# Optimization experiments

Hardware: AMD Instinct MI355X
Metric: run time of the kernel (lower is better)

## Reference

```python
import jax, jax.numpy as jnp
import numpy as np

NUM_HEADS = 16


def _rope(x, c, s):
    # x: [T, H, D]; c, s: [T, D/2] -> rotate-half RoPE over full head_dim
    d2 = c.shape[-1]
    x1, x2 = x[..., :d2], x[..., d2:]
    c = c[:, None, :]
    s = s[:, None, :]
    return jnp.concatenate([x1 * c - x2 * s, x2 * c + x1 * s], axis=-1)


def setup_inputs() -> dict:
    key = jax.random.key(0)
    ks = jax.random.split(key, 4)
    B, L, dim = 8, 1024, 1024
    T = B * L
    D = dim // NUM_HEADS
    hidden_states = jax.random.normal(ks[0], (T, dim), dtype=jnp.float32)
    w_qkv = jax.random.normal(ks[1], (dim, 3 * dim), dtype=jnp.float32) * (dim ** -0.5)
    b_qkv = jnp.zeros((3 * dim,), dtype=jnp.float32)
    w_proj = jax.random.normal(ks[2], (dim, dim), dtype=jnp.float32) * (dim ** -0.5)
    b_proj = jnp.zeros((dim,), dtype=jnp.float32)
    # RoPE tables: positions restart at 0 for each packed sequence
    pos = jnp.tile(jnp.arange(L, dtype=jnp.float32), B)  # [T]
    inv_freq = 1.0 / (10000.0 ** (jnp.arange(0, D, 2, dtype=jnp.float32) / D))  # [D/2]
    freqs = pos[:, None] * inv_freq[None, :]  # [T, D/2]
    emb = jnp.concatenate([freqs, freqs], axis=-1)  # [T, D]
    cos = jnp.cos(emb)
    sin = jnp.sin(emb)
    cu_seqlens = (jnp.arange(B + 1, dtype=jnp.int32) * L)
    return {"hidden_states": hidden_states, "cos": cos, "sin": sin,
            "w_qkv": w_qkv, "b_qkv": b_qkv, "w_proj": w_proj, "b_proj": b_proj,
            "cu_seqlens": cu_seqlens}


def reference(hidden_states, cos, sin, w_qkv, b_qkv, w_proj, b_proj, cu_seqlens):
    T, dim = hidden_states.shape
    H = NUM_HEADS
    D = dim // H
    B = cu_seqlens.shape[0] - 1  # equal-length packed sequences
    L = T // B

    qkv = hidden_states @ w_qkv + b_qkv            # [T, 3*dim]
    qkv = qkv.reshape(T, 3, H, D)
    q, k, v = qkv[:, 0], qkv[:, 1], qkv[:, 2]       # [T, H, D]

    # module chunks cos/sin in half along last dim before apply_rotary_emb
    c = cos[..., : D // 2].astype(jnp.float32)
    s = sin[..., : D // 2].astype(jnp.float32)
    q = _rope(q.astype(jnp.float32), c, s).astype(hidden_states.dtype)
    k = _rope(k.astype(jnp.float32), c, s).astype(hidden_states.dtype)

    # varlen flash attention == block-diagonal attention; equal lengths -> reshape
    qb = q.reshape(B, L, H, D)
    kb = k.reshape(B, L, H, D)
    vb = v.reshape(B, L, H, D)
    scale = D ** -0.5
    scores = jnp.einsum("bqhd,bkhd->bhqk", qb, kb) * scale  # [B, H, L, L]
    probs = jax.nn.softmax(scores, axis=-1)
    out = jnp.einsum("bhqk,bkhd->bqhd", probs, vb)           # [B, L, H, D]
    out = out.reshape(T, dim)
    return out @ w_proj + b_proj
```

## Files before the change

### kernel.cpp

```cpp
#include <hip/hip_runtime.h>

typedef unsigned short ushort_t;
typedef __attribute__((ext_vector_type(8))) short short8;
typedef __attribute__((ext_vector_type(4))) float f32x4;

#define AS1 __attribute__((address_space(1)))
#define AS3 __attribute__((address_space(3)))

__device__ __forceinline__ ushort_t f2bf(float f) {
  unsigned int u = __builtin_bit_cast(unsigned int, f);
  u += 0x7fffu + ((u >> 16) & 1u);
  return (ushort_t)(u >> 16);
}

__device__ __forceinline__ unsigned int pack_bf2(float a, float b) {
  unsigned int ua = __builtin_bit_cast(unsigned int, a) + 0x8000u;
  unsigned int ub = __builtin_bit_cast(unsigned int, b) + 0x8000u;
  return (ua >> 16) | (ub & 0xffff0000u);
}

#if defined(__has_builtin)
#if __has_builtin(__builtin_amdgcn_cvt_pk_bf16_f32)
#define HAVE_CVT_PK_BF16 1
#endif
#if __has_builtin(__builtin_amdgcn_exp2f)
#define HAVE_EXP2 1
#endif
#endif

__device__ __forceinline__ unsigned int pack2(float a, float b) {
#ifdef HAVE_CVT_PK_BF16
  typedef __attribute__((ext_vector_type(2))) __bf16 bf2_t;
  bf2_t r = __builtin_amdgcn_cvt_pk_bf16_f32(a, b);
  return __builtin_bit_cast(unsigned int, r);
#else
  return pack_bf2(a, b);
#endif
}

__device__ __forceinline__ float fast_exp2(float x) {
#ifdef HAVE_EXP2
  return __builtin_amdgcn_exp2f(x);
#else
  return exp2f(x);
#endif
}

__device__ __forceinline__ void load_lds16(const ushort_t* g, ushort_t* l) {
  __builtin_amdgcn_global_load_lds((AS1 void*)g, (AS3 void*)l, 16, 0, 0);
}

#define MFMA16(a, b, c) __builtin_amdgcn_mfma_f32_16x16x32_bf16((a), (b), (c), 0, 0, 0)

__global__ __launch_bounds__(256) void k_prep(const float* __restrict__ hs,
                                              ushort_t* __restrict__ hsb,
                                              const float* __restrict__ wqkv,
                                              ushort_t* __restrict__ wqkvT,
                                              const float* __restrict__ wproj,
                                              ushort_t* __restrict__ wprojT) {
  __shared__ __align__(16) ushort_t t[64 * 66];
  const int bid = blockIdx.x;
  if (bid < 4096) {
    int i = bid * 256 + threadIdx.x;
    const float4* s4 = (const float4*)hs;
    float4 a = s4[(size_t)i * 2], b = s4[(size_t)i * 2 + 1];
    short8 o;
    o[0] = (short)f2bf(a.x); o[1] = (short)f2bf(a.y);
    o[2] = (short)f2bf(a.z); o[3] = (short)f2bf(a.w);
    o[4] = (short)f2bf(b.x); o[5] = (short)f2bf(b.y);
    o[6] = (short)f2bf(b.z); o[7] = (short)f2bf(b.w);
    *(short8*)(hsb + (size_t)i * 8) = o;
    return;
  }
  const float* src;
  ushort_t* dst;
  int C, bx, by;
  if (bid < 4864) { int idx = bid - 4096; src = wqkv; dst = wqkvT; C = 3072;
                    bx = idx % 48; by = idx / 48; }
  else            { int idx = bid - 4864; src = wproj; dst = wprojT; C = 1024;
                    bx = idx & 15; by = idx >> 4; }
  const int R = 1024;
  const int x0 = bx * 64, y0 = by * 64;
  const int a2 = threadIdx.x & 31;
  const int r0 = threadIdx.x >> 5;
#pragma unroll
  for (int i = 0; i < 8; ++i) {
    int r = r0 + i * 8;
    float2 v = *(const float2*)&src[(size_t)(y0 + r) * C + x0 + 2 * a2];
    t[(2 * a2) * 66 + r]     = f2bf(v.x);
    t[(2 * a2 + 1) * 66 + r] = f2bf(v.y);
  }
  __syncthreads();
#pragma unroll
  for (int i = 0; i < 8; ++i) {
    int rr = r0 + i * 8;
    unsigned int w = *(const unsigned int*)&t[rr * 66 + 2 * a2];
    *(unsigned int*)&dst[(size_t)(x0 + rr) * R + y0 + 2 * a2] = w;
  }
}

__global__ __launch_bounds__(512) void k_qkv_gemm_rope(
    const ushort_t* __restrict__ A, const ushort_t* __restrict__ Bt,
    const float* __restrict__ bias, const float* __restrict__ cosb,
    const float* __restrict__ sinb, ushort_t* __restrict__ Qb,
    ushort_t* __restrict__ Kb, ushort_t* __restrict__ Vp) {
  constexpr int K = 1024;
  __shared__ __align__(16) ushort_t As[256 * 64];
  __shared__ __align__(16) ushort_t Bs[128 * 64];
  const int tid = threadIdx.x, lane = tid & 63, wave = tid >> 6;
  const int quad = lane >> 4, ml = lane & 15;
  const int wm = wave & 3, wn = wave >> 2;
  const int L = blockIdx.x, xcd = L & 7, j = L >> 3;
  const int by = xcd * 4 + j / 24, bx = j % 24;
  const int m0 = by * 256, n0 = bx * 128;
  f32x4 acc[4][4] = {};

  for (int kt = 0; kt < K / 64; ++kt) {
    __syncthreads();
    {
      const int kk0 = kt * 64;
#pragma unroll
      for (int i = 0; i < 4; ++i) {
        int cch = i * 512 + tid;
        int r = cch >> 3, s = cch & 7, gs = s ^ (r & 7);
        load_lds16(A + (size_t)(m0 + r) * K + kk0 + gs * 8, As + cch * 8);
      }
#pragma unroll
      for (int i = 0; i < 2; ++i) {
        int cch = i * 512 + tid;
        int r = cch >> 3, s = cch & 7, gs = s ^ (r & 7);
        load_lds16(Bt + (size_t)(n0 + r) * K + kk0 + gs * 8, Bs + cch * 8);
      }
    }
    __syncthreads();
#pragma unroll
    for (int ks = 0; ks < 2; ++ks) {
      short8 af[4], bfr[4];
#pragma unroll
      for (int mb = 0; mb < 4; ++mb) {
        int row = wm * 64 + mb * 16 + ml;
        int gs = (ks * 4 + quad) ^ (row & 7);
        af[mb] = *(const short8*)(As + row * 64 + gs * 8);
      }
#pragma unroll
      for (int nb = 0; nb < 4; ++nb) {
        int row = wn * 64 + nb * 16 + ml;
        int gs = (ks * 4 + quad) ^ (row & 7);
        bfr[nb] = *(const short8*)(Bs + row * 64 + gs * 8);
      }
#pragma unroll
      for (int mb = 0; mb < 4; ++mb)
#pragma unroll
        for (int nb = 0; nb < 4; ++nb)
          acc[mb][nb] = MFMA16(af[mb], bfr[nb], acc[mb][nb]);
    }
  }

  const int ncol0 = n0 + wn * 64;
  const int sec = ncol0 >> 10;
  const int h = (ncol0 & 1023) >> 6;
  if (sec < 2) {
    ushort_t* dst = (sec == 0) ? Qb : Kb;
    const float qs = (sec == 0) ? 0.18033688011112042f : 1.0f;
#pragma unroll
    for (int mb = 0; mb < 4; ++mb) {
#pragma unroll
      for (int rg = 0; rg < 4; ++rg) {
        const int m = m0 + wm * 64 + mb * 16 + quad * 4 + rg;
        const int b = m >> 10, l = m & 1023;
        const size_t ob = ((size_t)(b * 16 + h) * 1024 + l) * 64;
#pragma unroll
        for (int nb = 0; nb < 2; ++nb) {
          const int d = nb * 16 + ml;
          float x1 = acc[mb][nb][rg] + bias[ncol0 + d];
          float x2 = acc[mb][nb + 2][rg] + bias[ncol0 + d + 32];
          float cv = cosb[(size_t)m * 64 + d] * qs;
          float sv = sinb[(size_t)m * 64 + d] * qs;
          dst[ob + d] = f2bf(x1 * cv - x2 * sv);
          dst[ob + d + 32] = f2bf(x2 * cv + x1 * sv);
        }
      }
    }
  } else {
    const int mrow = m0 + wm * 64;
    const int b = mrow >> 10, lB = mrow & 1023;
    ushort_t* vb = Vp + ((size_t)(b * 16 + h)) * 65536 + lB;
#pragma unroll
    for (int rg = 0; rg < 4; ++rg) {
#pragma unroll
      for (int nb = 0; nb < 4; ++nb) {
        const int d = nb * 16 + ml;
        const float bs = bias[ncol0 + d];
        uint2 w;
        w.x = pack_bf2(acc[0][nb][rg] + bs, acc[1][nb][rg] + bs);
        w.y = pack_bf2(acc[2][nb][rg] + bs, acc[3][nb][rg] + bs);
        *(uint2*)(vb + (size_t)d * 1024 + 16 * quad + 4 * rg) = w;
      }
    }
  }
}

__global__ __launch_bounds__(512, 4) void k_attn(const ushort_t* __restrict__ Qb,
                                                 const ushort_t* __restrict__ Kb,
                                                 const ushort_t* __restrict__ Vp,
                                                 ushort_t* __restrict__ Ob) {
  __shared__ __align__(16) ushort_t S[32768];
  const int tid = threadIdx.x, lane = tid & 63, wave = tid >> 6;
  const int quad = lane >> 4, ml = lane & 15;
  const int bh = blockIdx.x & 127, qt = blockIdx.x >> 7;
  const int q0 = qt * 256;
  const size_t base = (size_t)bh * 65536;

#pragma unroll
  for (int i = 0; i < 4; ++i) {
    int cch = i * 512 + tid;
    int r = cch >> 3, s = cch & 7, gs = s ^ (r & 7);
    load_lds16(Qb + base + (size_t)(q0 + r) * 64 + gs * 8, S + cch * 8);
  }

  const ushort_t* kg;
  const ushort_t* vg;
  ushort_t *kl, *vl;
  {
    int r = tid >> 3, gs = (tid & 7) ^ (r & 7);
    kg = Kb + base + (size_t)r * 64 + gs * 8;
    kl = S + 16384 + tid * 8;
    vg = Vp + base + (size_t)r * 1024 + gs * 8;
    vl = S + 24576 + tid * 8;
  }
  load_lds16(kg, kl); kg += 4096;
  load_lds16(vg, vl); vg += 64;
  __syncthreads();

  const int gsA = quad ^ (ml & 7);
  const int gsB = (4 + quad) ^ (ml & 7);
  const int h0 = (ml >> 1) ^ (quad * 4);

  short8 qf[2][2];
#pragma unroll
  for (int mb = 0; mb < 2; ++mb) {
    int rowoff = wave * 2048 + mb * 1024 + ml * 64;
    qf[mb][0] = *(const short8*)(S + rowoff + gsA * 8);
    qf[mb][1] = *(const short8*)(S + rowoff + gsB * 8);
  }
  __syncthreads();

  const ushort_t* kA = S + 16384 + ml * 64 + gsA * 8;
  const ushort_t* kB = S + 16384 + ml * 64 + gsB * 8;
  const ushort_t* pA = S + wave * 2048 + ml * 64 + gsA * 8;
  const ushort_t* pB = S + wave * 2048 + ml * 64 + gsB * 8;
  ushort_t* pwl = S + wave * 2048 + quad * 256 + (ml & 1) * 4;

  f32x4 Oacc[2][4] = {};
  float lsum[2][4] = {};

#define ATTN_STEP(CUR, LAST)                                                  \
  {                                                                           \
    if (!(LAST)) {                                                            \
      load_lds16(kg, kl + ((CUR) ^ 1) * 4096); kg += 4096;                    \
      load_lds16(vg, vl + ((CUR) ^ 1) * 4096); vg += 64;                      \
    }                                                                         \
    f32x4 Sacc[2][4] = {};                                                    \
    __builtin_amdgcn_s_setprio(1);                                            \
    _Pragma("unroll") for (int nb = 0; nb < 4; ++nb) {                        \
      short8 kfa = *(const short8*)(kA + (CUR) * 4096 + nb * 1024);           \
      short8 kfb = *(const short8*)(kB + (CUR) * 4096 + nb * 1024);           \
      Sacc[0][nb] = MFMA16(qf[0][0], kfa, Sacc[0][nb]);                       \
      Sacc[1][nb] = MFMA16(qf[1][0], kfa, Sacc[1][nb]);                       \
      Sacc[0][nb] = MFMA16(qf[0][1], kfb, Sacc[0][nb]);                       \
      Sacc[1][nb] = MFMA16(qf[1][1], kfb, Sacc[1][nb]);                       \
    }                                                                         \
    __builtin_amdgcn_s_setprio(0);                                            \
    _Pragma("unroll") for (int mb = 0; mb < 2; ++mb) {                        \
      _Pragma("unroll") for (int rg = 0; rg < 4; ++rg) {                      \
        float p0 = fast_exp2(Sacc[mb][0][rg]);                                \
        float p1 = fast_exp2(Sacc[mb][1][rg]);                                \
        float p2 = fast_exp2(Sacc[mb][2][rg]);                                \
        float p3 = fast_exp2(Sacc[mb][3][rg]);                                \
        lsum[mb][rg] += (p0 + p1) + (p2 + p3);                                \
        uint2 w;                                                              \
        w.x = pack2(p0, p1);                                                  \
        w.y = pack2(p2, p3);                                                  \
        int g8 = ((h0 ^ rg) & 7) * 8;                                         \
        *(uint2*)(pwl + mb * 1024 + rg * 64 + g8) = w;                        \
      }                                                                       \
    }                                                                         \
    __builtin_amdgcn_s_setprio(1);                                            \
    _Pragma("unroll") for (int ks = 0; ks < 2; ++ks) {                        \
      const ushort_t* pk = ks ? pB : pA;                                      \
      const ushort_t* vk = (ks ? kB : kA) + 8192 + (CUR) * 4096;              \
      short8 pf0 = *(const short8*)(pk);                                      \
      short8 pf1 = *(const short8*)(pk + 1024);                               \
      _Pragma("unroll") for (int nb = 0; nb < 4; ++nb) {                      \
        short8 vf = *(const short8*)(vk + nb * 1024);                         \
        Oacc[0][nb] = MFMA16(pf0, vf, Oacc[0][nb]);                           \
        Oacc[1][nb] = MFMA16(pf1, vf, Oacc[1][nb]);                           \
      }                                                                       \
    }                                                                         \
    __builtin_amdgcn_s_setprio(0);                                            \
    __syncthreads();                                                          \
  }

#pragma unroll 1
  for (int kt2 = 0; kt2 < 8; ++kt2) {
    ATTN_STEP(0, false)
    ATTN_STEP(1, kt2 == 7)
  }
#undef ATTN_STEP

  const int b = bh >> 4, h = bh & 15;
#pragma unroll
  for (int mb = 0; mb < 2; ++mb) {
#pragma unroll
    for (int rg = 0; rg < 4; ++rg) {
      float l = lsum[mb][rg];
      l += __shfl_xor(l, 1);
      l += __shfl_xor(l, 2);
      l += __shfl_xor(l, 4);
      l += __shfl_xor(l, 8);
      float inv = 1.f / l;
      int q = q0 + wave * 32 + mb * 16 + quad * 4 + rg;
      size_t ob = ((size_t)(b * 1024 + q)) * 1024 + h * 64;
#pragma unroll
      for (int nb = 0; nb < 4; ++nb)
        Ob[ob + nb * 16 + ml] = f2bf(Oacc[mb][nb][rg] * inv);
    }
  }
}

__global__ __launch_bounds__(256) void k_proj_gemm(const ushort_t* __restrict__ A,
                                                   const ushort_t* __restrict__ Bt,
                                                   const float* __restrict__ bias,
                                                   float* __restrict__ out) {
  constexpr int K = 1024;
  __shared__ __align__(16) ushort_t As[128 * 128];
  __shared__ __align__(16) ushort_t Bs[128 * 128];
  const int tid = threadIdx.x, lane = tid & 63, wave = tid >> 6;
  const int quad = lane >> 4, ml = lane & 15;
  const int wm = wave & 1, wn = wave >> 1;
  const int L = blockIdx.x, xcd = L & 7, j = L >> 3;
  const int by = xcd * 8 + (j >> 3), bx = j & 7;
  const int m0 = by * 128, n0 = bx * 128;
  f32x4 acc[4][4] = {};

  for (int kt = 0; kt < K / 128; ++kt) {
    __syncthreads();
    {
      const int kk0 = kt * 128;
#pragma unroll
      for (int i = 0; i < 8; ++i) {
        int cch = i * 256 + tid;
        int r = cch >> 4, s = cch & 15, gs = s ^ (r & 15);
        load_lds16(A + (size_t)(m0 + r) * K + kk0 + gs * 8, As + cch * 8);
        load_lds16(Bt + (size_t)(n0 + r) * K + kk0 + gs * 8, Bs + cch * 8);
      }
    }
    __syncthreads();
#pragma unroll
    for (int ks = 0; ks < 4; ++ks) {
      short8 af[4], bfr[4];
#pragma unroll
      for (int mb = 0; mb < 4; ++mb) {
        int row = wm * 64 + mb * 16 + ml;
        int gs = (ks * 4 + quad) ^ (row & 15);
        af[mb] = *(const short8*)(As + row * 128 + gs * 8);
      }
#pragma unroll
      for (int nb = 0; nb < 4; ++nb) {
        int row = wn * 64 + nb * 16 + ml;
        int gs = (ks * 4 + quad) ^ (row & 15);
        bfr[nb] = *(const short8*)(Bs + row * 128 + gs * 8);
      }
#pragma unroll
      for (int mb = 0; mb < 4; ++mb)
#pragma unroll
        for (int nb = 0; nb < 4; ++nb)
          acc[mb][nb] = MFMA16(af[mb], bfr[nb], acc[mb][nb]);
    }
  }
#pragma unroll
  for (int mb = 0; mb < 4; ++mb) {
#pragma unroll
    for (int rg = 0; rg < 4; ++rg) {
      const int m = m0 + wm * 64 + mb * 16 + quad * 4 + rg;
#pragma unroll
      for (int nb = 0; nb < 4; ++nb) {
        const int n = n0 + wn * 64 + nb * 16 + ml;
        out[(size_t)m * 1024 + n] = acc[mb][nb][rg] + bias[n];
      }
    }
  }
}

extern "C" void kernel_launch(void* const* d_in, const int* in_sizes, int n_in,
                              void* d_out, int out_size, void* d_ws, size_t ws_size,
                              hipStream_t stream) {
  const float* hs = (const float*)d_in[0];
  const float* cosb = (const float*)d_in[1];
  const float* sinb = (const float*)d_in[2];
  const float* wqkv = (const float*)d_in[3];
  const float* bqkv = (const float*)d_in[4];
  const float* wproj = (const float*)d_in[5];
  const float* bproj = (const float*)d_in[6];
  float* out = (float*)d_out;

  char* ws = (char*)d_ws;
  ushort_t* hsb = (ushort_t*)(ws);
  ushort_t* wqkvT = (ushort_t*)(ws + (16u << 20));
  ushort_t* wprojT = (ushort_t*)(ws + (22u << 20));
  ushort_t* Qb = (ushort_t*)(ws + (24u << 20));
  ushort_t* Kb = (ushort_t*)(ws + (40u << 20));
  ushort_t* Vp = (ushort_t*)(ws + (56u << 20));
  ushort_t* attnb = hsb;

  k_prep<<<5120, 256, 0, stream>>>(hs, hsb, wqkv, wqkvT, wproj, wprojT);
  k_qkv_gemm_rope<<<768, 512, 0, stream>>>(hsb, wqkvT, bqkv, cosb, sinb,
                                           Qb, Kb, Vp);
  k_attn<<<512, 512, 0, stream>>>(Qb, Kb, Vp, attnb);
  k_proj_gemm<<<512, 256, 0, stream>>>(attnb, wprojT, bproj, out);
}
```

Before: 236.5 us.

## Load Q, K and V fragments directly from global memory instead of staging through LDS

The attention kernel stops staging Q, K and V tiles in shared memory with async LDS copies and a double buffer. Each wave now reads its MFMA operand fragments directly from global memory, and LDS is kept only for the per-wave probability tile. This removes the block-wide barriers and halves the LDS footprint, which may allow more resident blocks. The cost is exposed global-load latency inside the MFMA loop with no prefetching, plus redundant fetches of the same K/V data by all eight waves, which now rely on cache.

```diff
diff --git a/kernel.cpp b/kernel.cpp
--- a/kernel.cpp
+++ b/kernel.cpp
@@ -204,109 +204,83 @@
                                                  const ushort_t* __restrict__ Kb,
                                                  const ushort_t* __restrict__ Vp,
                                                  ushort_t* __restrict__ Ob) {
-  __shared__ __align__(16) ushort_t S[32768];
+  __shared__ __align__(16) ushort_t S[16384];
   const int tid = threadIdx.x, lane = tid & 63, wave = tid >> 6;
   const int quad = lane >> 4, ml = lane & 15;
   const int bh = blockIdx.x & 127, qt = blockIdx.x >> 7;
   const int q0 = qt * 256;
   const size_t base = (size_t)bh * 65536;
 
-#pragma unroll
-  for (int i = 0; i < 4; ++i) {
-    int cch = i * 512 + tid;
-    int r = cch >> 3, s = cch & 7, gs = s ^ (r & 7);
-    load_lds16(Qb + base + (size_t)(q0 + r) * 64 + gs * 8, S + cch * 8);
-  }
-
-  const ushort_t* kg;
-  const ushort_t* vg;
-  ushort_t *kl, *vl;
-  {
-    int r = tid >> 3, gs = (tid & 7) ^ (r & 7);
-    kg = Kb + base + (size_t)r * 64 + gs * 8;
-    kl = S + 16384 + tid * 8;
-    vg = Vp + base + (size_t)r * 1024 + gs * 8;
-    vl = S + 24576 + tid * 8;
-  }
-  load_lds16(kg, kl); kg += 4096;
-  load_lds16(vg, vl); vg += 64;
-  __syncthreads();
+  short8 qf[2][2];
+#pragma unroll
+  for (int mb = 0; mb < 2; ++mb)
+#pragma unroll
+    for (int ks = 0; ks < 2; ++ks)
+      qf[mb][ks] = *(const short8*)(Qb + base +
+          (size_t)(q0 + wave * 32 + mb * 16 + ml) * 64 + ks * 32 + quad * 8);
 
   const int gsA = quad ^ (ml & 7);
   const int gsB = (4 + quad) ^ (ml & 7);
   const int h0 = (ml >> 1) ^ (quad * 4);
-
-  short8 qf[2][2];
-#pragma unroll
-  for (int mb = 0; mb < 2; ++mb) {
-    int rowoff = wave * 2048 + mb * 1024 + ml * 64;
-    qf[mb][0] = *(const short8*)(S + rowoff + gsA * 8);
-    qf[mb][1] = *(const short8*)(S + rowoff + gsB * 8);
-  }
-  __syncthreads();
-
-  const ushort_t* kA = S + 16384 + ml * 64 + gsA * 8;
-  const ushort_t* kB = S + 16384 + ml * 64 + gsB * 8;
   const ushort_t* pA = S + wave * 2048 + ml * 64 + gsA * 8;
   const ushort_t* pB = S + wave * 2048 + ml * 64 + gsB * 8;
   ushort_t* pwl = S + wave * 2048 + quad * 256 + (ml & 1) * 4;
 
+  const ushort_t* kd = Kb + base + (size_t)ml * 64 + quad * 8;
+  const ushort_t* vd = Vp + base + (size_t)ml * 1024 + quad * 8;
+
   f32x4 Oacc[2][4] = {};
   float lsum[2][4] = {};
 
-#define ATTN_STEP(CUR, LAST)                                                  \
-  {                                                                           \
-    if (!(LAST)) {                                                            \
-      load_lds16(kg, kl + ((CUR) ^ 1) * 4096); kg += 4096;                    \
-      load_lds16(vg, vl + ((CUR) ^ 1) * 4096); vg += 64;                      \
-    }                                                                         \
-    f32x4 Sacc[2][4] = {};                                                    \
-    __builtin_amdgcn_s_setprio(1);                                            \
-    _Pragma("unroll") for (int nb = 0; nb < 4; ++nb) {                        \
-      short8 kfa = *(const short8*)(kA + (CUR) * 4096 + nb * 1024);           \
-      short8 kfb = *(const short8*)(kB + (CUR) * 4096 + nb * 1024);           \
-      Sacc[0][nb] = MFMA16(qf[0][0], kfa, Sacc[0][nb]);                       \
-      Sacc[1][nb] = MFMA16(qf[1][0], kfa, Sacc[1][nb]);                       \
-      Sacc[0][nb] = MFMA16(qf[0][1], kfb, Sacc[0][nb]);                       \
-      Sacc[1][nb] = MFMA16(qf[1][1], kfb, Sacc[1][nb]);                       \
-    }                                                                         \
-    __builtin_amdgcn_s_setprio(0);                                            \
-    _Pragma("unroll") for (int mb = 0; mb < 2; ++mb) {                        \
-      _Pragma("unroll") for (int rg = 0; rg < 4; ++rg) {                      \
-        float p0 = fast_exp2(Sacc[mb][0][rg]);                                \
-        float p1 = fast_exp2(Sacc[mb][1][rg]);                                \
-        float p2 = fast_exp2(Sacc[mb][2][rg]);                                \
-        float p3 = fast_exp2(Sacc[mb][3][rg]);                                \
-        lsum[mb][rg] += (p0 + p1) + (p2 + p3);                                \
-        uint2 w;                                                              \
-        w.x = pack2(p0, p1);                                                  \
-        w.y = pack2(p2, p3);                                                  \
-        int g8 = ((h0 ^ rg) & 7) * 8;                                         \
-        *(uint2*)(pwl + mb * 1024 + rg * 64 + g8) = w;                        \
-      }                                                                       \
-    }                                                                         \
-    __builtin_amdgcn_s_setprio(1);                                            \
-    _Pragma("unroll") for (int ks = 0; ks < 2; ++ks) {                        \
-      const ushort_t* pk = ks ? pB : pA;                                      \
-      const ushort_t* vk = (ks ? kB : kA) + 8192 + (CUR) * 4096;              \
-      short8 pf0 = *(const short8*)(pk);                                      \
-      short8 pf1 = *(const short8*)(pk + 1024);                               \
-      _Pragma("unroll") for (int nb = 0; nb < 4; ++nb) {                      \
-        short8 vf = *(const short8*)(vk + nb * 1024);                         \
-        Oacc[0][nb] = MFMA16(pf0, vf, Oacc[0][nb]);                           \
-        Oacc[1][nb] = MFMA16(pf1, vf, Oacc[1][nb]);                           \
-      }                                                                       \
-    }                                                                         \
-    __builtin_amdgcn_s_setprio(0);                                            \
-    __syncthreads();                                                          \
-  }
-
 #pragma unroll 1
-  for (int kt2 = 0; kt2 < 8; ++kt2) {
-    ATTN_STEP(0, false)
-    ATTN_STEP(1, kt2 == 7)
-  }
-#undef ATTN_STEP
+  for (int kt = 0; kt < 16; ++kt) {
+    f32x4 Sacc[2][4] = {};
+    __builtin_amdgcn_s_setprio(1);
+#pragma unroll
+    for (int nb = 0; nb < 4; ++nb) {
+      short8 kfa = *(const short8*)(kd + nb * 1024);
+      short8 kfb = *(const short8*)(kd + nb * 1024 + 32);
+      Sacc[0][nb] = MFMA16(qf[0][0], kfa, Sacc[0][nb]);
+      Sacc[1][nb] = MFMA16(qf[1][0], kfa, Sacc[1][nb]);
+      Sacc[0][nb] = MFMA16(qf[0][1], kfb, Sacc[0][nb]);
+      Sacc[1][nb] = MFMA16(qf[1][1], kfb, Sacc[1][nb]);
+    }
+    __builtin_amdgcn_s_setprio(0);
+    kd += 4096;
+
+#pragma unroll
+    for (int mb = 0; mb < 2; ++mb) {
+#pragma unroll
+      for (int rg = 0; rg < 4; ++rg) {
+        float p0 = fast_exp2(Sacc[mb][0][rg]);
+        float p1 = fast_exp2(Sacc[mb][1][rg]);
+        float p2 = fast_exp2(Sacc[mb][2][rg]);
+        float p3 = fast_exp2(Sacc[mb][3][rg]);
+        lsum[mb][rg] += (p0 + p1) + (p2 + p3);
+        uint2 w;
+        w.x = pack2(p0, p1);
+        w.y = pack2(p2, p3);
+        int g8 = ((h0 ^ rg) & 7) * 8;
+        *(uint2*)(pwl + mb * 1024 + rg * 64 + g8) = w;
+      }
+    }
+
+    __builtin_amdgcn_s_setprio(1);
+#pragma unroll
+    for (int ks = 0; ks < 2; ++ks) {
+      const ushort_t* pk = ks ? pB : pA;
+      short8 pf0 = *(const short8*)(pk);
+      short8 pf1 = *(const short8*)(pk + 1024);
+#pragma unroll
+      for (int nb = 0; nb < 4; ++nb) {
+        short8 vf = *(const short8*)(vd + (size_t)nb * 16384 + ks * 32);
+        Oacc[0][nb] = MFMA16(pf0, vf, Oacc[0][nb]);
+        Oacc[1][nb] = MFMA16(pf1, vf, Oacc[1][nb]);
+      }
+    }
+    __builtin_amdgcn_s_setprio(0);
+    vd += 64;
+  }
 
   const int b = bh >> 4, h = bh & 15;
 #pragma unroll
```

After: 306.6 us. 1.3x slower.
